# Performance work log

Hardware: AMD Instinct MI355X
Metric: run time of the kernel (lower is better)

Reference implementation:

```python
import jax, jax.numpy as jnp
import numpy as np

VOCAB, EMBED, HIDDEN, NCLASS = 50000, 256, 256, 5
B, T = 64, 512


def _lstm_cell(x, h, c, W, U, b):
    # Keras LSTMCell: gate order i, f, g(candidate), o
    z = x @ W + h @ U + b  # [B, 4H]
    i, f, g, o = jnp.split(z, 4, axis=-1)
    i = jax.nn.sigmoid(i)
    f = jax.nn.sigmoid(f)
    g = jnp.tanh(g)
    o = jax.nn.sigmoid(o)
    c_new = f * c + i * g
    h_new = o * jnp.tanh(c_new)
    return h_new, c_new


def _run_stacked(xs, W1, U1, b1, W2, U2, b2):
    # xs: [T, B, E] -> outputs of layer 2: [T, B, H]
    Bb = xs.shape[1]
    H = U1.shape[0]
    zero = jnp.zeros((Bb, H), dtype=xs.dtype)
    init = (zero, zero, zero, zero)

    def step(carry, x_t):
        h1, c1, h2, c2 = carry
        h1, c1 = _lstm_cell(x_t, h1, c1, W1, U1, b1)
        h2, c2 = _lstm_cell(h1, h2, c2, W2, U2, b2)
        return (h1, c1, h2, c2), h2

    _, ys = jax.lax.scan(step, init, xs)
    return ys


def setup_inputs() -> dict:
    key = jax.random.key(0)
    ks = jax.random.split(key, 16)
    s = 0.05

    def mk(k, shape):
        return (jax.random.normal(k, shape, dtype=jnp.float32) * s)

    inp = {
        "tokens": jax.random.randint(ks[0], (B, T), 0, VOCAB, dtype=jnp.int64),
        "embed_table": mk(ks[1], (VOCAB, EMBED)),
        # forward direction, layer 1 and 2
        "fw_W1": mk(ks[2], (EMBED, 4 * HIDDEN)),
        "fw_U1": mk(ks[3], (HIDDEN, 4 * HIDDEN)),
        "fw_b1": jnp.zeros((4 * HIDDEN,), jnp.float32),
        "fw_W2": mk(ks[4], (HIDDEN, 4 * HIDDEN)),
        "fw_U2": mk(ks[5], (HIDDEN, 4 * HIDDEN)),
        "fw_b2": jnp.zeros((4 * HIDDEN,), jnp.float32),
        # backward direction, layer 1 and 2
        "bw_W1": mk(ks[6], (EMBED, 4 * HIDDEN)),
        "bw_U1": mk(ks[7], (HIDDEN, 4 * HIDDEN)),
        "bw_b1": jnp.zeros((4 * HIDDEN,), jnp.float32),
        "bw_W2": mk(ks[8], (HIDDEN, 4 * HIDDEN)),
        "bw_U2": mk(ks[9], (HIDDEN, 4 * HIDDEN)),
        "bw_b2": jnp.zeros((4 * HIDDEN,), jnp.float32),
        # output dense (2H -> 5), softmax
        "dense_W": mk(ks[10], (2 * HIDDEN, NCLASS)),
        "dense_b": jnp.zeros((NCLASS,), jnp.float32),
    }
    return inp


def reference(tokens, embed_table,
              fw_W1, fw_U1, fw_b1, fw_W2, fw_U2, fw_b2,
              bw_W1, bw_U1, bw_b1, bw_W2, bw_U2, bw_b2,
              dense_W, dense_b):
    emb = embed_table[tokens]                    # [B, T, E]
    xs = jnp.swapaxes(emb, 0, 1)                 # [T, B, E]

    ys_fw = _run_stacked(xs, fw_W1, fw_U1, fw_b1, fw_W2, fw_U2, fw_b2)          # [T,B,H]
    ys_bw = _run_stacked(xs[::-1], bw_W1, bw_U1, bw_b1, bw_W2, bw_U2, bw_b2)[::-1]

    feat = jnp.concatenate([ys_fw, ys_bw], axis=-1)   # [T, B, 2H]
    feat = jnp.swapaxes(feat, 0, 1)                   # [B, T, 2H]
    logits = feat @ dense_W + dense_b                 # [B, T, 5]
    return jax.nn.softmax(logits, axis=-1)
```

## Files before the change

### kernel.cpp

```cpp
#include <hip/hip_runtime.h>

typedef __bf16 bf16;
typedef __bf16 bf16x8 __attribute__((ext_vector_type(8)));
typedef float f32x4 __attribute__((ext_vector_type(4)));
typedef unsigned long long u64;

#define T_LEN 512
#define BATCH 64
#define HID 256
#define LDA 520
#define ZLD 68

#define CTRL_BYTES 4096
#define H1_OFF CTRL_BYTES
#define HSLOT_U64 4096
#define HBUF_BYTES (2 * 3 * HSLOT_U64 * 8)
#define H2_OFF (H1_OFF + HBUF_BYTES)
#define LOG_OFF (H2_OFF + HBUF_BYTES)
#define LOG_BYTES (T_LEN * BATCH * 5 * 4)
#define ZERO_BYTES (LOG_OFF + LOG_BYTES)

#define SMEM_A 66560
#define SMEM_Z 17408
#define SMEM_C 4096
#define SMEM_TAIL 576
#define SMEM_BYTES (SMEM_A + SMEM_Z + SMEM_C + SMEM_TAIL)

__device__ inline uint4 cvt8(const float4* s) {
    float4 a = s[0], b = s[1];
    union { uint4 u; bf16 h[8]; } r;
    r.h[0] = (bf16)a.x; r.h[1] = (bf16)a.y; r.h[2] = (bf16)a.z; r.h[3] = (bf16)a.w;
    r.h[4] = (bf16)b.x; r.h[5] = (bf16)b.y; r.h[6] = (bf16)b.z; r.h[7] = (bf16)b.w;
    return r.u;
}

__global__ void __launch_bounds__(256, 1)
lstm_kernel(const int* __restrict__ tokens,
            const float* __restrict__ embed,
            const float* __restrict__ W1f, const float* __restrict__ U1f, const float* __restrict__ b1f,
            const float* __restrict__ W2f, const float* __restrict__ U2f, const float* __restrict__ b2f,
            const float* __restrict__ W1b, const float* __restrict__ U1b, const float* __restrict__ b1b,
            const float* __restrict__ W2b, const float* __restrict__ U2b, const float* __restrict__ b2b,
            const float* __restrict__ dW,
            char* __restrict__ ws)
{
    extern __shared__ char smem[];
    bf16*  Abuf  = (bf16*)smem;
    float* zLds  = (float*)(smem + SMEM_A);
    float* cLds  = (float*)(smem + SMEM_A + SMEM_Z);
    float* bLds  = (float*)(smem + SMEM_A + SMEM_Z + SMEM_C);
    float* dwLds = bLds + 64;

    const int tid = threadIdx.x;
    const int wg  = blockIdx.x;
    const int dir = wg & 1, layer = (wg >> 1) & 1, sub = wg >> 2;

    const float *Wp, *Up, *bp;
    if (dir == 0) { if (layer == 0) { Wp=W1f; Up=U1f; bp=b1f; } else { Wp=W2f; Up=U2f; bp=b2f; } }
    else          { if (layer == 0) { Wp=W1b; Up=U1b; bp=b1b; } else { Wp=W2b; Up=U2b; bp=b2b; } }

    {
        for (int it = 0; it < 32; ++it) {
            int idx = it * 256 + tid;
            int k = idx >> 4, q4 = idx & 15;
            int g = q4 >> 2, u0 = (q4 & 3) * 4;
            const float* src = (k < 256) ? (Wp + (size_t)k * 1024 + g * 256 + sub * 16 + u0)
                                         : (Up + (size_t)(k - 256) * 1024 + g * 256 + sub * 16 + u0);
            float4 v = *(const float4*)src;
            int c0 = g * 16 + u0;
            Abuf[(c0 + 0) * LDA + k] = (bf16)v.x;
            Abuf[(c0 + 1) * LDA + k] = (bf16)v.y;
            Abuf[(c0 + 2) * LDA + k] = (bf16)v.z;
            Abuf[(c0 + 3) * LDA + k] = (bf16)v.w;
        }
        if (tid < 64) {
            int g = tid >> 4, u = tid & 15;
            bLds[tid] = bp[g * 256 + sub * 16 + u];
        }
        if (tid < 80) {
            int u = tid / 5, c = tid % 5;
            dwLds[tid] = dW[(size_t)(dir * 256 + sub * 16 + u) * 5 + c];
        }
        for (int i = tid; i < 1024; i += 256) cLds[i] = 0.f;
    }
    __syncthreads();

    const int wave = tid >> 6, lane = tid & 63, quad = lane >> 4, ln = lane & 15;
    const int mrow0 = (wave >> 1) * 32, ncol0 = (wave & 1) * 32;
    bf16x8 bfrag[2][16];
#pragma unroll
    for (int nt = 0; nt < 2; ++nt)
#pragma unroll
        for (int kt = 0; kt < 16; ++kt)
            bfrag[nt][kt] = *(const bf16x8*)&Abuf[(ncol0 + nt * 16 + ln) * LDA + kt * 32 + quad * 8];
    __syncthreads();

    u64* h1buf = (u64*)(ws + H1_OFF) + (size_t)dir * 3 * HSLOT_U64;
    u64* h2buf = (u64*)(ws + H2_OFF) + (size_t)dir * 3 * HSLOT_U64;
    u64* hOwn  = (layer == 0) ? h1buf : h2buf;
    float* logits   = (float*)(ws + LOG_OFF);
    unsigned* ctrOwn = (unsigned*)ws + (dir * 2 + layer) * 32;
    unsigned* ctrL1  = (unsigned*)ws + (dir * 2 + 0) * 32;
    unsigned* ctrL2  = (unsigned*)ws + (dir * 2 + 1) * 32;

    const int bA = tid >> 2, qA = tid & 3;

    float4 pf[16];
    int tokB = 0;
    if (layer == 0) {
        const int tt0 = dir ? (T_LEN - 1) : 0;
        int tokA = tokens[bA * T_LEN + tt0];
        const float4* src = (const float4*)(embed + (size_t)tokA * HID + qA * 64);
#pragma unroll
        for (int j = 0; j < 16; ++j) pf[j] = src[j];
        const int tt1 = dir ? (T_LEN - 2) : 1;
        tokB = tokens[bA * T_LEN + tt1];
    }

    for (int s = 0; s < T_LEN; ++s) {
        if (tid == 0) {
            unsigned needOwn = (unsigned)s * 16u;
            while (__hip_atomic_load(ctrOwn, __ATOMIC_RELAXED, __HIP_MEMORY_SCOPE_AGENT) < needOwn) {}
            if (layer == 0 && s >= 3) {
                unsigned needT = (unsigned)(s - 2) * 16u;
                while (__hip_atomic_load(ctrL2, __ATOMIC_RELAXED, __HIP_MEMORY_SCOPE_AGENT) < needT) {}
            }
        }
        __syncthreads();

        u64 hreg[16];
        {
            const u64* hsrc = hOwn + (size_t)(s % 3) * HSLOT_U64;
#pragma unroll
            for (int k = 0; k < 16; ++k)
                hreg[k] = __hip_atomic_load(hsrc + k * 256 + tid, __ATOMIC_RELAXED, __HIP_MEMORY_SCOPE_AGENT);
        }
        if (layer == 0) {
            uint4* dstx = (uint4*)&Abuf[bA * LDA + qA * 64];
#pragma unroll
            for (int j = 0; j < 8; ++j) dstx[j] = cvt8(&pf[2 * j]);
        } else {
            if (tid == 0) {
                unsigned needX = (unsigned)(s + 1) * 16u;
                while (__hip_atomic_load(ctrL1, __ATOMIC_RELAXED, __HIP_MEMORY_SCOPE_AGENT) < needX) {}
            }
            __syncthreads();
            u64 xreg[16];
            const u64* xsrc = h1buf + (size_t)((s + 1) % 3) * HSLOT_U64;
#pragma unroll
            for (int k = 0; k < 16; ++k)
                xreg[k] = __hip_atomic_load(xsrc + k * 256 + tid, __ATOMIC_RELAXED, __HIP_MEMORY_SCOPE_AGENT);
#pragma unroll
            for (int k = 0; k < 16; ++k)
                *(u64*)&Abuf[bA * LDA + k * 16 + qA * 4] = xreg[k];
        }
#pragma unroll
        for (int k = 0; k < 16; ++k)
            *(u64*)&Abuf[bA * LDA + 256 + k * 16 + qA * 4] = hreg[k];
        __syncthreads();

        if (layer == 0) {
            const float4* src = (const float4*)(embed + (size_t)tokB * HID + qA * 64);
#pragma unroll
            for (int j = 0; j < 16; ++j) pf[j] = src[j];
            const int sn2 = (s + 2 < T_LEN) ? s + 2 : T_LEN - 1;
            const int tt2 = dir ? (T_LEN - 1 - sn2) : sn2;
            tokB = tokens[bA * T_LEN + tt2];
        }

        f32x4 acc[2][2];
#pragma unroll
        for (int mi = 0; mi < 2; ++mi)
#pragma unroll
            for (int ni = 0; ni < 2; ++ni) acc[mi][ni] = (f32x4)(0.0f);
#pragma unroll
        for (int kt = 0; kt < 16; ++kt) {
            bf16x8 a0 = *(const bf16x8*)&Abuf[(mrow0 + ln) * LDA + kt * 32 + quad * 8];
            bf16x8 a1 = *(const bf16x8*)&Abuf[(mrow0 + 16 + ln) * LDA + kt * 32 + quad * 8];
            acc[0][0] = __builtin_amdgcn_mfma_f32_16x16x32_bf16(a0, bfrag[0][kt], acc[0][0], 0, 0, 0);
            acc[0][1] = __builtin_amdgcn_mfma_f32_16x16x32_bf16(a0, bfrag[1][kt], acc[0][1], 0, 0, 0);
            acc[1][0] = __builtin_amdgcn_mfma_f32_16x16x32_bf16(a1, bfrag[0][kt], acc[1][0], 0, 0, 0);
            acc[1][1] = __builtin_amdgcn_mfma_f32_16x16x32_bf16(a1, bfrag[1][kt], acc[1][1], 0, 0, 0);
        }
#pragma unroll
        for (int mi = 0; mi < 2; ++mi)
#pragma unroll
            for (int ni = 0; ni < 2; ++ni) {
                int row = mrow0 + mi * 16 + quad * 4;
                int col = ncol0 + ni * 16 + ln;
#pragma unroll
                for (int r = 0; r < 4; ++r)
                    zLds[(row + r) * ZLD + col] = acc[mi][ni][r];
            }
        __syncthreads();

        u64* hdst = hOwn + (size_t)((s + 1) % 3) * HSLOT_U64;
        float hv[4];
        {
            const int b = bA, u0 = qA * 4;
#pragma unroll
            for (int e = 0; e < 4; ++e) {
                int u = u0 + e;
                float zi = zLds[b * ZLD + u]      + bLds[u];
                float zf = zLds[b * ZLD + 16 + u] + bLds[16 + u];
                float zg = zLds[b * ZLD + 32 + u] + bLds[32 + u];
                float zo = zLds[b * ZLD + 48 + u] + bLds[48 + u];
                float ig = 1.f / (1.f + __expf(-zi));
                float fg = 1.f / (1.f + __expf(-zf));
                float gg = 1.f - 2.f / (__expf(2.f * zg) + 1.f);
                float og = 1.f / (1.f + __expf(-zo));
                float cn = fg * cLds[b * 16 + u] + ig * gg;
                cLds[b * 16 + u] = cn;
                hv[e] = og * (1.f - 2.f / (__expf(2.f * cn) + 1.f));
            }
            union { u64 w; bf16 h[4]; } pk;
#pragma unroll
            for (int e = 0; e < 4; ++e) pk.h[e] = (bf16)hv[e];
            __hip_atomic_store(hdst + sub * 256 + tid, pk.w,
                               __ATOMIC_RELAXED, __HIP_MEMORY_SCOPE_AGENT);
        }
        float pr[5];
        if (layer == 1) {
#pragma unroll
            for (int c = 0; c < 5; ++c)
                pr[c] = hv[0] * dwLds[(qA * 4 + 0) * 5 + c] + hv[1] * dwLds[(qA * 4 + 1) * 5 + c]
                      + hv[2] * dwLds[(qA * 4 + 2) * 5 + c] + hv[3] * dwLds[(qA * 4 + 3) * 5 + c];
#pragma unroll
            for (int m = 1; m < 4; m <<= 1)
#pragma unroll
                for (int c = 0; c < 5; ++c) pr[c] += __shfl_xor(pr[c], m);
        }

        asm volatile("s_waitcnt vmcnt(0)" ::: "memory");
        __syncthreads();
        if (tid == 0)
            __hip_atomic_fetch_add(ctrOwn, 1u, __ATOMIC_RELAXED, __HIP_MEMORY_SCOPE_AGENT);

        if (layer == 1 && qA == 0) {
            const int tp = dir ? (T_LEN - 1 - s) : s;
            float* lp = &logits[((size_t)tp * BATCH + bA) * 5];
#pragma unroll
            for (int c = 0; c < 5; ++c) atomicAdd(lp + c, pr[c]);
        }
    }
}

__global__ void __launch_bounds__(256)
softmax_kernel(const char* __restrict__ ws, const float* __restrict__ dB, float* __restrict__ out)
{
    const int gid = blockIdx.x * 256 + threadIdx.x;
    const int b = gid & 63, t = gid >> 6;
    const float* lp = (const float*)(ws + LOG_OFF) + ((size_t)t * BATCH + b) * 5;
    float l[5];
#pragma unroll
    for (int c = 0; c < 5; ++c) l[c] = lp[c] + dB[c];
    float m = l[0];
#pragma unroll
    for (int c = 1; c < 5; ++c) m = fmaxf(m, l[c]);
    float e[5], ssum = 0.f;
#pragma unroll
    for (int c = 0; c < 5; ++c) { e[c] = __expf(l[c] - m); ssum += e[c]; }
    float inv = 1.f / ssum;
    float* o = out + ((size_t)b * T_LEN + t) * 5;
#pragma unroll
    for (int c = 0; c < 5; ++c) o[c] = e[c] * inv;
}

extern "C" void kernel_launch(void* const* d_in, const int* in_sizes, int n_in,
                              void* d_out, int out_size, void* d_ws, size_t ws_size,
                              hipStream_t stream)
{
    const int*   tokens = (const int*)d_in[0];
    const float* embed  = (const float*)d_in[1];
    const float* W1f = (const float*)d_in[2],  *U1f = (const float*)d_in[3],  *b1f = (const float*)d_in[4];
    const float* W2f = (const float*)d_in[5],  *U2f = (const float*)d_in[6],  *b2f = (const float*)d_in[7];
    const float* W1b = (const float*)d_in[8],  *U1b = (const float*)d_in[9],  *b1b = (const float*)d_in[10];
    const float* W2b = (const float*)d_in[11], *U2b = (const float*)d_in[12], *b2b = (const float*)d_in[13];
    const float* dW  = (const float*)d_in[14], *dB  = (const float*)d_in[15];

    hipFuncSetAttribute(reinterpret_cast<const void*>(lstm_kernel),
                        hipFuncAttributeMaxDynamicSharedMemorySize, SMEM_BYTES);
    hipMemsetAsync(d_ws, 0, ZERO_BYTES, stream);
    lstm_kernel<<<dim3(64), dim3(256), SMEM_BYTES, stream>>>(
        tokens, embed, W1f, U1f, b1f, W2f, U2f, b2f,
        W1b, U1b, b1b, W2b, U2b, b2b, dW, (char*)d_ws);
    softmax_kernel<<<dim3(128), dim3(256), 0, stream>>>((const char*)d_ws, dB, (float*)d_out);
}
```

Measured before the change: 3.090 ms.

## Replace counter-based handoff with epoch-tagged flag-in-data ring buffers

```diff
diff --git a/kernel.cpp b/kernel.cpp
--- a/kernel.cpp
+++ b/kernel.cpp
@@ -12,13 +12,13 @@
 #define ZLD 68
 
 #define CTRL_BYTES 4096
-#define H1_OFF CTRL_BYTES
+#define LOG_OFF CTRL_BYTES
+#define LOG_BYTES (T_LEN * BATCH * 5 * 4)
+#define RING_OFF (LOG_OFF + LOG_BYTES)
 #define HSLOT_U64 4096
-#define HBUF_BYTES (2 * 3 * HSLOT_U64 * 8)
-#define H2_OFF (H1_OFF + HBUF_BYTES)
-#define LOG_OFF (H2_OFF + HBUF_BYTES)
-#define LOG_BYTES (T_LEN * BATCH * 5 * 4)
-#define ZERO_BYTES (LOG_OFF + LOG_BYTES)
+#define RING_SLOTS 16
+#define RING_U64 (RING_SLOTS * HSLOT_U64)
+#define RING_BYTES (4 * RING_U64 * 8)
 
 #define SMEM_A 66560
 #define SMEM_Z 17408
@@ -32,6 +32,25 @@
     r.h[0] = (bf16)a.x; r.h[1] = (bf16)a.y; r.h[2] = (bf16)a.z; r.h[3] = (bf16)a.w;
     r.h[4] = (bf16)b.x; r.h[5] = (bf16)b.y; r.h[6] = (bf16)b.z; r.h[7] = (bf16)b.w;
     return r.u;
+}
+
+__device__ __forceinline__ void poll16(const u64* src, int tid, unsigned ep, u64* dst) {
+    unsigned todo = 0xffffu;
+#pragma unroll
+    for (int k = 0; k < 16; ++k)
+        dst[k] = __hip_atomic_load(src + k * 256 + tid, __ATOMIC_RELAXED, __HIP_MEMORY_SCOPE_AGENT);
+    for (;;) {
+        unsigned rem = 0u;
+#pragma unroll
+        for (int k = 0; k < 16; ++k)
+            if (((todo >> k) & 1u) && (((unsigned)dst[k]) & 1u) != ep) rem |= (1u << k);
+        if (!rem) break;
+        todo = rem;
+#pragma unroll
+        for (int k = 0; k < 16; ++k)
+            if ((todo >> k) & 1u)
+                dst[k] = __hip_atomic_load(src + k * 256 + tid, __ATOMIC_RELAXED, __HIP_MEMORY_SCOPE_AGENT);
+    }
 }
 
 __global__ void __launch_bounds__(256, 1)
@@ -95,15 +114,14 @@
             bfrag[nt][kt] = *(const bf16x8*)&Abuf[(ncol0 + nt * 16 + ln) * LDA + kt * 32 + quad * 8];
     __syncthreads();
 
-    u64* h1buf = (u64*)(ws + H1_OFF) + (size_t)dir * 3 * HSLOT_U64;
-    u64* h2buf = (u64*)(ws + H2_OFF) + (size_t)dir * 3 * HSLOT_U64;
-    u64* hOwn  = (layer == 0) ? h1buf : h2buf;
-    float* logits   = (float*)(ws + LOG_OFF);
-    unsigned* ctrOwn = (unsigned*)ws + (dir * 2 + layer) * 32;
-    unsigned* ctrL1  = (unsigned*)ws + (dir * 2 + 0) * 32;
-    unsigned* ctrL2  = (unsigned*)ws + (dir * 2 + 1) * 32;
+    u64* ringL1  = (u64*)(ws + RING_OFF) + (size_t)(dir * 2 + 0) * RING_U64;
+    u64* ringL2  = (u64*)(ws + RING_OFF) + (size_t)(dir * 2 + 1) * RING_U64;
+    u64* ringOwn = (layer == 0) ? ringL1 : ringL2;
+    float* logits  = (float*)(ws + LOG_OFF);
+    unsigned* prog = (unsigned*)ws + dir * 32;
 
     const int bA = tid >> 2, qA = tid & 3;
+    unsigned progCache = 0u;
 
     float4 pf[16];
     int tokB = 0;
@@ -118,38 +136,29 @@
     }
 
     for (int s = 0; s < T_LEN; ++s) {
-        if (tid == 0) {
-            unsigned needOwn = (unsigned)s * 16u;
-            while (__hip_atomic_load(ctrOwn, __ATOMIC_RELAXED, __HIP_MEMORY_SCOPE_AGENT) < needOwn) {}
-            if (layer == 0 && s >= 3) {
-                unsigned needT = (unsigned)(s - 2) * 16u;
-                while (__hip_atomic_load(ctrL2, __ATOMIC_RELAXED, __HIP_MEMORY_SCOPE_AGENT) < needT) {}
-            }
-        }
-        __syncthreads();
+        if (layer == 0 && tid == 0 && s >= 13) {
+            unsigned need = (unsigned)(s - 12);
+            while (progCache < need)
+                progCache = __hip_atomic_load(prog, __ATOMIC_RELAXED, __HIP_MEMORY_SCOPE_AGENT);
+        }
 
         u64 hreg[16];
-        {
-            const u64* hsrc = hOwn + (size_t)(s % 3) * HSLOT_U64;
-#pragma unroll
-            for (int k = 0; k < 16; ++k)
-                hreg[k] = __hip_atomic_load(hsrc + k * 256 + tid, __ATOMIC_RELAXED, __HIP_MEMORY_SCOPE_AGENT);
-        }
+        if (s == 0) {
+#pragma unroll
+            for (int k = 0; k < 16; ++k) hreg[k] = 0ull;
+        } else {
+            poll16(ringOwn + (size_t)(s & 15) * HSLOT_U64, tid,
+                   (unsigned)(((s - 1) >> 4) & 1), hreg);
+        }
+
         if (layer == 0) {
             uint4* dstx = (uint4*)&Abuf[bA * LDA + qA * 64];
 #pragma unroll
             for (int j = 0; j < 8; ++j) dstx[j] = cvt8(&pf[2 * j]);
         } else {
-            if (tid == 0) {
-                unsigned needX = (unsigned)(s + 1) * 16u;
-                while (__hip_atomic_load(ctrL1, __ATOMIC_RELAXED, __HIP_MEMORY_SCOPE_AGENT) < needX) {}
-            }
-            __syncthreads();
             u64 xreg[16];
-            const u64* xsrc = h1buf + (size_t)((s + 1) % 3) * HSLOT_U64;
-#pragma unroll
-            for (int k = 0; k < 16; ++k)
-                xreg[k] = __hip_atomic_load(xsrc + k * 256 + tid, __ATOMIC_RELAXED, __HIP_MEMORY_SCOPE_AGENT);
+            poll16(ringL1 + (size_t)((s + 1) & 15) * HSLOT_U64, tid,
+                   (unsigned)((s >> 4) & 1), xreg);
 #pragma unroll
             for (int k = 0; k < 16; ++k)
                 *(u64*)&Abuf[bA * LDA + k * 16 + qA * 4] = xreg[k];
@@ -194,7 +203,7 @@
             }
         __syncthreads();
 
-        u64* hdst = hOwn + (size_t)((s + 1) % 3) * HSLOT_U64;
+        u64* hdst = ringOwn + (size_t)((s + 1) & 15) * HSLOT_U64;
         float hv[4];
         {
             const int b = bA, u0 = qA * 4;
@@ -216,6 +225,7 @@
             union { u64 w; bf16 h[4]; } pk;
 #pragma unroll
             for (int e = 0; e < 4; ++e) pk.h[e] = (bf16)hv[e];
+            pk.w = (pk.w & ~1ull) | (u64)((s >> 4) & 1);
             __hip_atomic_store(hdst + sub * 256 + tid, pk.w,
                                __ATOMIC_RELAXED, __HIP_MEMORY_SCOPE_AGENT);
         }
@@ -231,10 +241,9 @@
                 for (int c = 0; c < 5; ++c) pr[c] += __shfl_xor(pr[c], m);
         }
 
-        asm volatile("s_waitcnt vmcnt(0)" ::: "memory");
-        __syncthreads();
-        if (tid == 0)
-            __hip_atomic_fetch_add(ctrOwn, 1u, __ATOMIC_RELAXED, __HIP_MEMORY_SCOPE_AGENT);
+        if (layer == 1 && tid == 0)
+            __hip_atomic_store(prog, (unsigned)(s + 1),
+                               __ATOMIC_RELAXED, __HIP_MEMORY_SCOPE_AGENT);
 
         if (layer == 1 && qA == 0) {
             const int tp = dir ? (T_LEN - 1 - s) : s;
@@ -280,7 +289,8 @@
 
     hipFuncSetAttribute(reinterpret_cast<const void*>(lstm_kernel),
                         hipFuncAttributeMaxDynamicSharedMemorySize, SMEM_BYTES);
-    hipMemsetAsync(d_ws, 0, ZERO_BYTES, stream);
+    hipMemsetAsync(d_ws, 0, RING_OFF, stream);
+    hipMemsetAsync((char*)d_ws + RING_OFF, 0xFF, RING_BYTES, stream);
     lstm_kernel<<<dim3(64), dim3(256), SMEM_BYTES, stream>>>(
         tokens, embed, W1f, U1f, b1f, W2f, U2f, b2f,
         W1b, U1b, b1b, W2b, U2b, b2b, dW, (char*)d_ws);
```

Measured after the change: 3.423 ms. +10.8%, slower.
